# Kernel tuning notes

Hardware: AMD Instinct MI355X
Metric: run time of the kernel (lower is better)

## Reference

```python
import jax, jax.numpy as jnp
import numpy as np

# SplineConv (PyG), dim=1, kernel_size=2, degree=1, open spline, aggr='mean',
# root_weight=True, bias=True.
# For K=2, m=1, dim=1 the B-spline basis per edge reduces exactly to
#   basis = (1 - u, u) with kernel indices (0, 1), u = edge_attr[:, 0] in [0, 1].

N_NODES = 50000
N_EDGES = 1600000
D_IN = 128
D_OUT = 128


def setup_inputs() -> dict:
    key = jax.random.key(0)
    k1, k2, k3, k4, k5, k6, k7 = jax.random.split(key, 7)
    x = jax.random.normal(k1, (N_NODES, D_IN), dtype=jnp.float32)
    edge_index = jax.random.randint(k2, (2, N_EDGES), 0, N_NODES, dtype=jnp.int64)
    edge_attr = jax.random.uniform(k3, (N_EDGES, 1), dtype=jnp.float32)
    # Glorot-ish init for spline weights [K^dim=2, D_IN, D_OUT]
    scale = 1.0 / np.sqrt(D_IN)
    W = jax.random.normal(k4, (2, D_IN, D_OUT), dtype=jnp.float32) * scale
    W_root = jax.random.normal(k5, (D_IN, D_OUT), dtype=jnp.float32) * scale
    bias = jax.random.normal(k6, (D_OUT,), dtype=jnp.float32) * 0.01
    return {"x": x, "edge_index": edge_index, "edge_attr": edge_attr,
            "W": W, "W_root": W_root, "bias": bias}


def reference(x, edge_index, edge_attr, W, W_root, bias):
    n = x.shape[0]
    src, dst = edge_index[0], edge_index[1]
    u = jnp.clip(edge_attr[:, 0], 0.0, 1.0)          # [E]
    # Node-level GEMMs for both kernel weight slots (cheaper than per-edge GEMM)
    h = jnp.einsum('nd,kde->kne', x, W)              # [2, N, D_OUT]
    # Per-edge spline-weighted message: (1-u)*h0[src] + u*h1[src]
    msg = (1.0 - u)[:, None] * h[0][src] + u[:, None] * h[1][src]  # [E, D_OUT]
    agg = jax.ops.segment_sum(msg, dst, num_segments=n)            # [N, D_OUT]
    deg = jax.ops.segment_sum(jnp.ones_like(u), dst, num_segments=n)
    agg = agg / jnp.maximum(deg, 1.0)[:, None]       # mean aggregation
    return agg + x @ W_root + bias
```

## Files before the change

### kernel.cpp

```cpp
#include <hip/hip_runtime.h>

static constexpr int N = 50000;
static constexpr int E = 1600000;
static constexpr int D = 128;
static constexpr int NB = (N + 63) / 64;
static constexpr int BIN_BLKS = 256;
static constexpr int CHUNK = E / BIN_BLKS;
static constexpr int SLOTS = (CHUNK + 1023) / 1024;
static constexpr int BKT_CAP = 3072;
static constexpr int CVT_BLKS = (N * D / 8 + 1023) / 1024;
static constexpr int W_BLKS = 48;

typedef __attribute__((ext_vector_type(8))) short short8;
typedef __attribute__((ext_vector_type(4))) float f32x4;
typedef __attribute__((ext_vector_type(2))) float f32x2;

__device__ __forceinline__ uint bf16rne2(float a, float b) {
    uint ua = __float_as_uint(a), ub = __float_as_uint(b);
    ua += 0x7fffu + ((ua >> 16) & 1u);
    ub += 0x7fffu + ((ub >> 16) & 1u);
    return (ua >> 16) | (ub & 0xffff0000u);
}

__device__ __forceinline__ void gload16(const void* g, void* l) {
    __builtin_amdgcn_global_load_lds(
        (const __attribute__((address_space(1))) void*)g,
        (__attribute__((address_space(3))) void*)l, 16, 0, 0);
}

__device__ __forceinline__ int logical_blk() {
    return (blockIdx.x & 7) * (BIN_BLKS / 8) + (blockIdx.x >> 3);
}

__global__ __launch_bounds__(1024) void binprep_k(
        const int* __restrict__ ei, const float* __restrict__ ea,
        const float* __restrict__ x, const float* __restrict__ W,
        const float* __restrict__ Wr, int* __restrict__ gcur,
        uint* __restrict__ pay, ushort* __restrict__ xb,
        uchar* __restrict__ xf8, ushort* __restrict__ Wt) {
    __shared__ int hist[NB];
    __shared__ int pfx[NB];
    __shared__ int base[NB];
    __shared__ uint srtpay[CHUNK];
    __shared__ int  srtpos[CHUNK];
    __shared__ int wsum[16];
    __shared__ int tot_s;
    int t = threadIdx.x;
    int lane = t & 63, wv = t >> 6;
    if (blockIdx.x < BIN_BLKS) {
        int b = logical_blk();
        if (t < NB) hist[t] = 0;
        __syncthreads();
        int b0 = b * CHUNK;
        uint mypay[SLOTS];
        int  mybkt[SLOTS];
        int  myrank[SLOTS];
#pragma unroll
        for (int k = 0; k < SLOTS; ++k) {
            int i = b0 + t + k * 1024;
            myrank[k] = -1;
            if (t + k * 1024 < CHUNK) {
                int dst = ei[E + i];
                if ((unsigned)dst < (unsigned)N) {
                    int src = ei[i];
                    float u = fminf(fmaxf(ea[i], 0.0f), 1.0f);
                    uint u10 = (uint)(u * 1023.0f + 0.5f);
                    int bkt = dst >> 6;
                    mybkt[k] = bkt;
                    mypay[k] = (u10 << 22) | ((uint)(dst & 63) << 16) | (uint)src;
                    myrank[k] = atomicAdd(&hist[bkt], 1);
                }
            }
        }
        __syncthreads();
        int c = (t < NB) ? hist[t] : 0;
        int s = c;
#pragma unroll
        for (int d = 1; d < 64; d <<= 1) {
            int o = __shfl_up(s, d);
            if (lane >= d) s += o;
        }
        if (lane == 63) wsum[wv] = s;
        __syncthreads();
        if (t < 16) {
            int v = wsum[t];
            int si = v;
#pragma unroll
            for (int d = 1; d < 16; d <<= 1) {
                int o = __shfl_up(si, d);
                if (t >= d) si += o;
            }
            wsum[t] = si - v;
            if (t == 15) tot_s = si;
        }
        __syncthreads();
        int excl = s - c + wsum[wv];
        if (t < NB) {
            pfx[t] = excl;
            base[t] = c ? atomicAdd(&gcur[t], c) : 0;
        }
        __syncthreads();
#pragma unroll
        for (int k = 0; k < SLOTS; ++k) {
            if (myrank[k] >= 0) {
                int bk = mybkt[k];
                int slot = pfx[bk] + myrank[k];
                srtpay[slot] = mypay[k];
                int p = base[bk] + myrank[k];
                srtpos[slot] = (p < BKT_CAP) ? (bk * BKT_CAP + p) : -1;
            }
        }
        __syncthreads();
        int tot = tot_s;
        for (int i = t; i < tot; i += 1024) {
            int pos = srtpos[i];
            if (pos >= 0) pay[pos] = srtpay[i];
        }
    } else if (blockIdx.x < BIN_BLKS + CVT_BLKS) {
        int i = (blockIdx.x - BIN_BLKS) * 1024 + t;
        if (i < N * D / 8) {
            float4 v0 = ((const float4*)x)[2 * i];
            float4 v1 = ((const float4*)x)[2 * i + 1];
            uint4 ob = { bf16rne2(v0.x, v0.y), bf16rne2(v0.z, v0.w),
                         bf16rne2(v1.x, v1.y), bf16rne2(v1.z, v1.w) };
            ((uint4*)xb)[i] = ob;
            int lo = __builtin_amdgcn_cvt_pk_fp8_f32(v0.x, v0.y, 0, false);
            lo = __builtin_amdgcn_cvt_pk_fp8_f32(v0.z, v0.w, lo, true);
            int hi = __builtin_amdgcn_cvt_pk_fp8_f32(v1.x, v1.y, 0, false);
            hi = __builtin_amdgcn_cvt_pk_fp8_f32(v1.z, v1.w, hi, true);
            uint2 o8 = { (uint)lo, (uint)hi };
            ((uint2*)xf8)[i] = o8;
        }
    } else {
        int i = (blockIdx.x - BIN_BLKS - CVT_BLKS) * 1024 + t;
        int n = i / 384, r = i % 384;
        float v = (r < 256) ? W[(size_t)r * 128 + n]
                            : Wr[(size_t)(r - 256) * 128 + n];
        uint u = __float_as_uint(v);
        u += 0x7fffu + ((u >> 16) & 1u);
        Wt[(size_t)n * 384 + r] = (ushort)(u >> 16);
    }
}

__global__ __launch_bounds__(1024) void sortagg_k(
        const uchar* __restrict__ xf8, const int* __restrict__ gcur,
        const uint* __restrict__ pay, ushort* __restrict__ a0b,
        ushort* __restrict__ a1b) {
    __shared__ uint srt[BKT_CAP];
    __shared__ int hist[64];
    __shared__ int off64[65];
    int b = blockIdx.x, t = threadIdx.x;
    int beg = b * BKT_CAP;
    int c = gcur[b];
    if (c > BKT_CAP) c = BKT_CAP;
    if (t < 64) hist[t] = 0;
    __syncthreads();
    uint mypay[3]; int myrank[3];
#pragma unroll
    for (int k = 0; k < 3; ++k) {
        int i = t + k * 1024;
        if (i < c) {
            uint p = pay[beg + i];
            mypay[k] = p;
            myrank[k] = atomicAdd(&hist[(p >> 16) & 63], 1);
        }
    }
    __syncthreads();
    if (t < 64) {
        int v = hist[t];
        int s = v;
        for (int d = 1; d < 64; d <<= 1) {
            int o = __shfl_up(s, d);
            if (t >= d) s += o;
        }
        off64[t] = s - v;
        if (t == 63) off64[64] = s;
    }
    __syncthreads();
#pragma unroll
    for (int k = 0; k < 3; ++k) {
        int i = t + k * 1024;
        if (i < c) {
            uint p = mypay[k];
            srt[off64[(p >> 16) & 63] + myrank[k]] = p;
        }
    }
    __syncthreads();

    int lane = t & 63;
    int wv   = t >> 6;
    int grp  = (lane >> 4);
    int cl   = lane & 15;
    int nloc = wv * 4 + grp;
    int s0 = off64[nloc], s1 = off64[nloc + 1];
    int deg = s1 - s0;

    f32x2 S[4], T[4];
#pragma unroll
    for (int q = 0; q < 4; ++q) { S[q] = 0.f; T[q] = 0.f; }

    int j = s0;
    for (; j + 3 < s1; j += 4) {
        uint p[4];
        uint2 v[4];
#pragma unroll
        for (int d = 0; d < 4; ++d) p[d] = srt[j + d];
#pragma unroll
        for (int d = 0; d < 4; ++d)
            v[d] = *(const uint2*)(xf8 + (size_t)(p[d] & 0xffffu) * D + cl * 8);
#pragma unroll
        for (int d = 0; d < 4; ++d) {
            float u = (float)(p[d] >> 22) * (1.0f / 1023.0f);
            f32x2 u2 = {u, u};
            f32x2 xv0 = __builtin_amdgcn_cvt_pk_f32_fp8((int)v[d].x, false);
            f32x2 xv1 = __builtin_amdgcn_cvt_pk_f32_fp8((int)v[d].x, true);
            f32x2 xv2 = __builtin_amdgcn_cvt_pk_f32_fp8((int)v[d].y, false);
            f32x2 xv3 = __builtin_amdgcn_cvt_pk_f32_fp8((int)v[d].y, true);
            S[0] += xv0; T[0] = u2 * xv0 + T[0];
            S[1] += xv1; T[1] = u2 * xv1 + T[1];
            S[2] += xv2; T[2] = u2 * xv2 + T[2];
            S[3] += xv3; T[3] = u2 * xv3 + T[3];
        }
    }
    for (; j < s1; ++j) {
        uint p0 = srt[j];
        uint2 v0 = *(const uint2*)(xf8 + (size_t)(p0 & 0xffffu) * D + cl * 8);
        float u = (float)(p0 >> 22) * (1.0f / 1023.0f);
        f32x2 u2 = {u, u};
        f32x2 xv0 = __builtin_amdgcn_cvt_pk_f32_fp8((int)v0.x, false);
        f32x2 xv1 = __builtin_amdgcn_cvt_pk_f32_fp8((int)v0.x, true);
        f32x2 xv2 = __builtin_amdgcn_cvt_pk_f32_fp8((int)v0.y, false);
        f32x2 xv3 = __builtin_amdgcn_cvt_pk_f32_fp8((int)v0.y, true);
        S[0] += xv0; T[0] = u2 * xv0 + T[0];
        S[1] += xv1; T[1] = u2 * xv1 + T[1];
        S[2] += xv2; T[2] = u2 * xv2 + T[2];
        S[3] += xv3; T[3] = u2 * xv3 + T[3];
    }

    int node = b * 64 + nloc;
    if (node < N) {
        float inv = 1.0f / fmaxf((float)deg, 1.0f);
        uint4 oa = { bf16rne2((S[0].x - T[0].x) * inv, (S[0].y - T[0].y) * inv),
                     bf16rne2((S[1].x - T[1].x) * inv, (S[1].y - T[1].y) * inv),
                     bf16rne2((S[2].x - T[2].x) * inv, (S[2].y - T[2].y) * inv),
                     bf16rne2((S[3].x - T[3].x) * inv, (S[3].y - T[3].y) * inv) };
        uint4 ob = { bf16rne2(T[0].x * inv, T[0].y * inv),
                     bf16rne2(T[1].x * inv, T[1].y * inv),
                     bf16rne2(T[2].x * inv, T[2].y * inv),
                     bf16rne2(T[3].x * inv, T[3].y * inv) };
        *(uint4*)(a0b + (size_t)node * D + cl * 8) = oa;
        *(uint4*)(a1b + (size_t)node * D + cl * 8) = ob;
    }
}

__global__ __launch_bounds__(256) void gemm_k(
        const ushort* __restrict__ a0b, const ushort* __restrict__ a1b,
        const ushort* __restrict__ xb, const ushort* __restrict__ Wt,
        const float* __restrict__ bias, float* __restrict__ out) {
    __shared__ ushort As[128 * 64];
    __shared__ ushort Bs[128 * 64];

    int t    = threadIdx.x;
    int lane = t & 63;
    int w    = t >> 6;
    int r2   = w >> 1, c2 = w & 1;
    int q    = lane >> 4;
    int l16  = lane & 15;
    int row0 = blockIdx.x * 128;
    int rsub  = lane >> 3;
    int cslot = lane & 7;
    int xorc  = cslot ^ rsub;

    f32x4 acc[4][4];
#pragma unroll
    for (int i = 0; i < 4; ++i)
#pragma unroll
        for (int j = 0; j < 4; ++j) acc[i][j] = 0.f;

    const ushort* Asrc[3] = {a0b, a1b, xb};

#pragma unroll
    for (int kt = 0; kt < 384; kt += 64) {
        const ushort* Ab = Asrc[kt >> 7];
        int ko = kt & 127;
#pragma unroll
        for (int h = 0; h < 4; ++h) {
            int region = h * 4 + w;
            int r = region * 8 + rsub;
            int ra = row0 + r; ra = ra < N ? ra : N - 1;
            gload16(Ab + (size_t)ra * 128 + ko + xorc * 8, As + region * 512);
            gload16(Wt + (size_t)r * 384 + kt + xorc * 8,  Bs + region * 512);
        }
        __syncthreads();
#pragma unroll
        for (int kk = 0; kk < 2; ++kk) {
            short8 af[4], bf[4];
#pragma unroll
            for (int mt = 0; mt < 4; ++mt) {
                int r = r2 * 64 + mt * 16 + l16;
                int slot = (kk * 4 + q) ^ (r & 7);
                af[mt] = *(const short8*)&As[r * 64 + slot * 8];
            }
#pragma unroll
            for (int nt = 0; nt < 4; ++nt) {
                int n = c2 * 64 + nt * 16 + l16;
                int slot = (kk * 4 + q) ^ (n & 7);
                bf[nt] = *(const short8*)&Bs[n * 64 + slot * 8];
            }
#pragma unroll
            for (int mt = 0; mt < 4; ++mt)
#pragma unroll
                for (int nt = 0; nt < 4; ++nt)
                    acc[mt][nt] = __builtin_amdgcn_mfma_f32_16x16x32_bf16(
                        af[mt], bf[nt], acc[mt][nt], 0, 0, 0);
        }
        __syncthreads();
    }

#pragma unroll
    for (int nt = 0; nt < 4; ++nt) {
        int col = c2 * 64 + nt * 16 + l16;
        float bb = bias[col];
#pragma unroll
        for (int mt = 0; mt < 4; ++mt) {
#pragma unroll
            for (int r = 0; r < 4; ++r) {
                int row = row0 + r2 * 64 + mt * 16 + q * 4 + r;
                if (row < N) out[(size_t)row * 128 + col] = acc[mt][nt][r] + bb;
            }
        }
    }
}

extern "C" void kernel_launch(void* const* d_in, const int* in_sizes, int n_in,
                              void* d_out, int out_size, void* d_ws, size_t ws_size,
                              hipStream_t stream) {
    const float* x    = (const float*)d_in[0];
    const int*   ei   = (const int*)d_in[1];
    const float* ea   = (const float*)d_in[2];
    const float* W    = (const float*)d_in[3];
    const float* Wr   = (const float*)d_in[4];
    const float* bias = (const float*)d_in[5];
    float* out = (float*)d_out;

    char* ws = (char*)d_ws;
    size_t o = 0;
    auto alloc = [&](size_t bytes) -> void* {
        void* p = ws + o;
        o = (o + bytes + 255) & ~(size_t)255;
        return p;
    };
    int*    gcur = (int*)alloc((size_t)NB * 4);
    uint*   pay  = (uint*)alloc((size_t)NB * BKT_CAP * 4);
    ushort* xb   = (ushort*)alloc((size_t)N * D * 2);
    uchar*  xf8  = (uchar*)alloc((size_t)N * D);
    ushort* a0b  = (ushort*)alloc((size_t)N * D * 2);
    ushort* a1b  = (ushort*)alloc((size_t)N * D * 2);
    ushort* Wt   = (ushort*)alloc((size_t)128 * 384 * 2);
    (void)ws_size; (void)in_sizes; (void)n_in; (void)out_size;

    hipMemsetAsync(gcur, 0, (size_t)NB * 4, stream);
    binprep_k<<<BIN_BLKS + CVT_BLKS + W_BLKS, 1024, 0, stream>>>(
                 ei, ea, x, W, Wr, gcur, pay, xb, xf8, Wt);
    sortagg_k<<<NB, 1024, 0, stream>>>(xf8, gcur, pay, a0b, a1b);
    gemm_k   <<<(N + 127) / 128, 256, 0, stream>>>(a0b, a1b, xb, Wt, bias, out);
}
```

Baseline: 159.1 us.

## Split each node's edges across two 8-lane groups with 16-byte fp8 gathers

The sort-aggregate kernel now has 8 lanes read 16 bytes of the fp8 feature row each, instead of 16 lanes reading 8 bytes. Each node's edge list is split between two lane groups, and their partial sums are combined with xor shuffles before one group writes the result. The payload loads and output stores use nontemporal hints. The goal is fewer, wider gather instructions and more edge-level parallelism per node, at the cost of twice the accumulator registers and an extra shuffle reduction.

```diff
diff --git a/kernel.cpp b/kernel.cpp
--- a/kernel.cpp
+++ b/kernel.cpp
@@ -14,6 +14,7 @@
 typedef __attribute__((ext_vector_type(8))) short short8;
 typedef __attribute__((ext_vector_type(4))) float f32x4;
 typedef __attribute__((ext_vector_type(2))) float f32x2;
+typedef __attribute__((ext_vector_type(4))) uint u32x4;
 
 __device__ __forceinline__ uint bf16rne2(float a, float b) {
     uint ua = __float_as_uint(a), ub = __float_as_uint(b);
@@ -160,7 +161,7 @@
     for (int k = 0; k < 3; ++k) {
         int i = t + k * 1024;
         if (i < c) {
-            uint p = pay[beg + i];
+            uint p = __builtin_nontemporal_load(&pay[beg + i]);
             mypay[k] = p;
             myrank[k] = atomicAdd(&hist[(p >> 16) & 63], 1);
         }
@@ -189,67 +190,106 @@
 
     int lane = t & 63;
     int wv   = t >> 6;
-    int grp  = (lane >> 4);
-    int cl   = lane & 15;
-    int nloc = wv * 4 + grp;
+    int grp8 = lane >> 3;
+    int cl8  = lane & 7;
+    int gid  = wv * 8 + grp8;
+    int nloc = gid >> 1;
+    int half = gid & 1;
     int s0 = off64[nloc], s1 = off64[nloc + 1];
     int deg = s1 - s0;
-
-    f32x2 S[4], T[4];
-#pragma unroll
-    for (int q = 0; q < 4; ++q) { S[q] = 0.f; T[q] = 0.f; }
-
-    int j = s0;
-    for (; j + 3 < s1; j += 4) {
+    int mid = s0 + ((deg + 1) >> 1);
+    int js = half ? mid : s0;
+    int je = half ? s1 : mid;
+
+    f32x2 S[8], T[8];
+#pragma unroll
+    for (int q = 0; q < 8; ++q) { S[q] = 0.f; T[q] = 0.f; }
+
+    int j = js;
+    for (; j + 3 < je; j += 4) {
         uint p[4];
-        uint2 v[4];
+        u32x4 v[4];
 #pragma unroll
         for (int d = 0; d < 4; ++d) p[d] = srt[j + d];
 #pragma unroll
         for (int d = 0; d < 4; ++d)
-            v[d] = *(const uint2*)(xf8 + (size_t)(p[d] & 0xffffu) * D + cl * 8);
+            v[d] = *(const u32x4*)(xf8 + (size_t)(p[d] & 0xffffu) * D + cl8 * 16);
 #pragma unroll
         for (int d = 0; d < 4; ++d) {
             float u = (float)(p[d] >> 22) * (1.0f / 1023.0f);
             f32x2 u2 = {u, u};
-            f32x2 xv0 = __builtin_amdgcn_cvt_pk_f32_fp8((int)v[d].x, false);
-            f32x2 xv1 = __builtin_amdgcn_cvt_pk_f32_fp8((int)v[d].x, true);
-            f32x2 xv2 = __builtin_amdgcn_cvt_pk_f32_fp8((int)v[d].y, false);
-            f32x2 xv3 = __builtin_amdgcn_cvt_pk_f32_fp8((int)v[d].y, true);
-            S[0] += xv0; T[0] = u2 * xv0 + T[0];
-            S[1] += xv1; T[1] = u2 * xv1 + T[1];
-            S[2] += xv2; T[2] = u2 * xv2 + T[2];
-            S[3] += xv3; T[3] = u2 * xv3 + T[3];
-        }
-    }
-    for (; j < s1; ++j) {
+            f32x2 x0 = __builtin_amdgcn_cvt_pk_f32_fp8((int)v[d].x, false);
+            f32x2 x1 = __builtin_amdgcn_cvt_pk_f32_fp8((int)v[d].x, true);
+            f32x2 x2 = __builtin_amdgcn_cvt_pk_f32_fp8((int)v[d].y, false);
+            f32x2 x3 = __builtin_amdgcn_cvt_pk_f32_fp8((int)v[d].y, true);
+            f32x2 x4 = __builtin_amdgcn_cvt_pk_f32_fp8((int)v[d].z, false);
+            f32x2 x5 = __builtin_amdgcn_cvt_pk_f32_fp8((int)v[d].z, true);
+            f32x2 x6 = __builtin_amdgcn_cvt_pk_f32_fp8((int)v[d].w, false);
+            f32x2 x7 = __builtin_amdgcn_cvt_pk_f32_fp8((int)v[d].w, true);
+            S[0] += x0; T[0] = u2 * x0 + T[0];
+            S[1] += x1; T[1] = u2 * x1 + T[1];
+            S[2] += x2; T[2] = u2 * x2 + T[2];
+            S[3] += x3; T[3] = u2 * x3 + T[3];
+            S[4] += x4; T[4] = u2 * x4 + T[4];
+            S[5] += x5; T[5] = u2 * x5 + T[5];
+            S[6] += x6; T[6] = u2 * x6 + T[6];
+            S[7] += x7; T[7] = u2 * x7 + T[7];
+        }
+    }
+    for (; j < je; ++j) {
         uint p0 = srt[j];
-        uint2 v0 = *(const uint2*)(xf8 + (size_t)(p0 & 0xffffu) * D + cl * 8);
+        u32x4 v0 = *(const u32x4*)(xf8 + (size_t)(p0 & 0xffffu) * D + cl8 * 16);
         float u = (float)(p0 >> 22) * (1.0f / 1023.0f);
         f32x2 u2 = {u, u};
-        f32x2 xv0 = __builtin_amdgcn_cvt_pk_f32_fp8((int)v0.x, false);
-        f32x2 xv1 = __builtin_amdgcn_cvt_pk_f32_fp8((int)v0.x, true);
-        f32x2 xv2 = __builtin_amdgcn_cvt_pk_f32_fp8((int)v0.y, false);
-        f32x2 xv3 = __builtin_amdgcn_cvt_pk_f32_fp8((int)v0.y, true);
-        S[0] += xv0; T[0] = u2 * xv0 + T[0];
-        S[1] += xv1; T[1] = u2 * xv1 + T[1];
-        S[2] += xv2; T[2] = u2 * xv2 + T[2];
-        S[3] += xv3; T[3] = u2 * xv3 + T[3];
+        f32x2 x0 = __builtin_amdgcn_cvt_pk_f32_fp8((int)v0.x, false);
+        f32x2 x1 = __builtin_amdgcn_cvt_pk_f32_fp8((int)v0.x, true);
+        f32x2 x2 = __builtin_amdgcn_cvt_pk_f32_fp8((int)v0.y, false);
+        f32x2 x3 = __builtin_amdgcn_cvt_pk_f32_fp8((int)v0.y, true);
+        f32x2 x4 = __builtin_amdgcn_cvt_pk_f32_fp8((int)v0.z, false);
+        f32x2 x5 = __builtin_amdgcn_cvt_pk_f32_fp8((int)v0.z, true);
+        f32x2 x6 = __builtin_amdgcn_cvt_pk_f32_fp8((int)v0.w, false);
+        f32x2 x7 = __builtin_amdgcn_cvt_pk_f32_fp8((int)v0.w, true);
+        S[0] += x0; T[0] = u2 * x0 + T[0];
+        S[1] += x1; T[1] = u2 * x1 + T[1];
+        S[2] += x2; T[2] = u2 * x2 + T[2];
+        S[3] += x3; T[3] = u2 * x3 + T[3];
+        S[4] += x4; T[4] = u2 * x4 + T[4];
+        S[5] += x5; T[5] = u2 * x5 + T[5];
+        S[6] += x6; T[6] = u2 * x6 + T[6];
+        S[7] += x7; T[7] = u2 * x7 + T[7];
+    }
+
+#pragma unroll
+    for (int q = 0; q < 8; ++q) {
+        S[q].x += __shfl_xor(S[q].x, 8);
+        S[q].y += __shfl_xor(S[q].y, 8);
+        T[q].x += __shfl_xor(T[q].x, 8);
+        T[q].y += __shfl_xor(T[q].y, 8);
     }
 
     int node = b * 64 + nloc;
-    if (node < N) {
+    if (half == 0 && node < N) {
         float inv = 1.0f / fmaxf((float)deg, 1.0f);
-        uint4 oa = { bf16rne2((S[0].x - T[0].x) * inv, (S[0].y - T[0].y) * inv),
-                     bf16rne2((S[1].x - T[1].x) * inv, (S[1].y - T[1].y) * inv),
-                     bf16rne2((S[2].x - T[2].x) * inv, (S[2].y - T[2].y) * inv),
-                     bf16rne2((S[3].x - T[3].x) * inv, (S[3].y - T[3].y) * inv) };
-        uint4 ob = { bf16rne2(T[0].x * inv, T[0].y * inv),
-                     bf16rne2(T[1].x * inv, T[1].y * inv),
-                     bf16rne2(T[2].x * inv, T[2].y * inv),
-                     bf16rne2(T[3].x * inv, T[3].y * inv) };
-        *(uint4*)(a0b + (size_t)node * D + cl * 8) = oa;
-        *(uint4*)(a1b + (size_t)node * D + cl * 8) = ob;
+        u32x4 oa_lo = { bf16rne2((S[0].x - T[0].x) * inv, (S[0].y - T[0].y) * inv),
+                        bf16rne2((S[1].x - T[1].x) * inv, (S[1].y - T[1].y) * inv),
+                        bf16rne2((S[2].x - T[2].x) * inv, (S[2].y - T[2].y) * inv),
+                        bf16rne2((S[3].x - T[3].x) * inv, (S[3].y - T[3].y) * inv) };
+        u32x4 oa_hi = { bf16rne2((S[4].x - T[4].x) * inv, (S[4].y - T[4].y) * inv),
+                        bf16rne2((S[5].x - T[5].x) * inv, (S[5].y - T[5].y) * inv),
+                        bf16rne2((S[6].x - T[6].x) * inv, (S[6].y - T[6].y) * inv),
+                        bf16rne2((S[7].x - T[7].x) * inv, (S[7].y - T[7].y) * inv) };
+        u32x4 ob_lo = { bf16rne2(T[0].x * inv, T[0].y * inv),
+                        bf16rne2(T[1].x * inv, T[1].y * inv),
+                        bf16rne2(T[2].x * inv, T[2].y * inv),
+                        bf16rne2(T[3].x * inv, T[3].y * inv) };
+        u32x4 ob_hi = { bf16rne2(T[4].x * inv, T[4].y * inv),
+                        bf16rne2(T[5].x * inv, T[5].y * inv),
+                        bf16rne2(T[6].x * inv, T[6].y * inv),
+                        bf16rne2(T[7].x * inv, T[7].y * inv) };
+        __builtin_nontemporal_store(oa_lo, (u32x4*)(a0b + (size_t)node * D + cl8 * 16));
+        __builtin_nontemporal_store(oa_hi, (u32x4*)(a0b + (size_t)node * D + cl8 * 16 + 8));
+        __builtin_nontemporal_store(ob_lo, (u32x4*)(a1b + (size_t)node * D + cl8 * 16));
+        __builtin_nontemporal_store(ob_hi, (u32x4*)(a1b + (size_t)node * D + cl8 * 16 + 8));
     }
 }
 
```

Result: slower. 164.1 us (+3.2%).
